# Optimization experiments

Hardware: AMD Instinct MI355X
Metric: run time of the kernel (lower is better)

Reference implementation:

```python
import jax, jax.numpy as jnp
import numpy as np

BS, GRID, A, CH = 32, 2704, 3, 85   # 52x52 YOLO grid, 3 anchors, 80 classes + 5
HW = 52
VDIM, H, SEL = 1024, 512, 32
EPS = 1e-8


def setup_inputs() -> dict:
    key = jax.random.key(0)
    ks = jax.random.split(key, 16)
    s = 0.02
    return {
        "boxes": jax.random.uniform(ks[0], (BS, GRID, A, CH), dtype=jnp.float32),
        "x_feat": jax.random.normal(ks[1], (BS, VDIM, HW, HW), dtype=jnp.float32),
        "tag_emb": jax.random.normal(ks[2], (BS, SEL, H), dtype=jnp.float32),
        "pos_emb": jax.random.normal(ks[3], (BS, SEL, H), dtype=jnp.float32),
        "lang": jax.random.normal(ks[4], (BS, H), dtype=jnp.float32),
        "W_vs": jax.random.normal(ks[5], (VDIM, H), dtype=jnp.float32) * s,
        "b_vs": jnp.zeros((H,), jnp.float32),
        "W_ts": jax.random.normal(ks[6], (H, H), dtype=jnp.float32) * s,
        "b_ts": jnp.zeros((H,), jnp.float32),
        "W_vs_pos": jax.random.normal(ks[7], (H, H), dtype=jnp.float32) * s,
        "b_vs_pos": jnp.zeros((H,), jnp.float32),
        "W_tag": jax.random.normal(ks[8], (H, H), dtype=jnp.float32) * s,
        "b_tag": jnp.zeros((H,), jnp.float32),
        "W_soft": jax.random.normal(ks[9], (H, 2), dtype=jnp.float32) * s,
        "b_soft": jnp.zeros((2,), jnp.float32),
    }


def reference(boxes, x_feat, tag_emb, pos_emb, lang,
              W_vs, b_vs, W_ts, b_ts, W_vs_pos, b_vs_pos,
              W_tag, b_tag, W_soft, b_soft):
    bs = boxes.shape[0]
    # --- topk grid selection on mean objectness (channel 4) ---
    score = jnp.mean(boxes, axis=2)[:, :, 4]                     # [bs, grid]
    _, idx = jax.lax.top_k(score, SEL)                           # [bs, SEL]
    # torch's scatter->masked_select recovers selected grids in ascending
    # index order (not topk-value order), so sort the indices.
    idx = jnp.sort(idx, axis=1)
    # gather selected boxes: [bs, SEL, A, CH]
    boxes_sel = jnp.take_along_axis(boxes, idx[:, :, None, None], axis=1)
    # gather selected visual features: [bs, SEL, VDIM]
    feat = x_feat.reshape(bs, VDIM, -1).transpose(0, 2, 1)       # [bs, grid, VDIM]
    i_sel = jnp.take_along_axis(feat, idx[:, :, None], axis=1)
    # --- gated multimodal fusion ---
    vis = i_sel @ W_vs + b_vs                                    # [bs, SEL, H]
    lang_e = (lang @ W_ts + b_ts)[:, None, :]                    # [bs, 1, H]
    logits = ((vis + tag_emb + pos_emb) @ W_soft + b_soft) / 0.03
    w = jax.nn.log_softmax(logits, axis=-1)                      # [bs, SEL, 2]
    vis2 = ((vis * w[..., 0:1]) @ W_vs_pos + b_vs_pos
            + (tag_emb * w[..., 1:2]) @ W_tag + b_tag
            + pos_emb)                                           # [bs, SEL, H]
    # --- head (eval): cosine similarity vs language, top-1 grid mask ---
    vn = vis2 / (jnp.linalg.norm(vis2, axis=-1, keepdims=True) + EPS)
    ln = lang_e / (jnp.linalg.norm(lang_e, axis=-1, keepdims=True) + EPS)
    sim = jnp.sum(vn * ln, axis=-1)                              # [bs, SEL]
    top_grid = jnp.argmax(sim, axis=1)                           # [bs]
    # --- get_boxes: gather top grid, xywh->xyxy, top-1 box by objectness ---
    sel = jnp.take_along_axis(boxes_sel, top_grid[:, None, None, None], axis=1)
    sel = jax.lax.stop_gradient(sel[:, 0])                       # [bs, A, CH] (.data in torch)
    x1 = sel[..., 0] - sel[..., 2] / 2
    y1 = sel[..., 1] - sel[..., 3] / 2
    x2 = x1 + sel[..., 2]
    y2 = y1 + sel[..., 3]
    bxyxy = jnp.concatenate(
        [jnp.stack([x1, y1, x2, y2], axis=-1), sel[..., 4:]], axis=-1)
    j = jnp.argmax(bxyxy[:, :, 4], axis=1)                       # [bs]
    box_pred = jnp.take_along_axis(bxyxy[:, :, :5], j[:, None, None], axis=1)
    return box_pred, sim
```

## Files before the change

kernel.cpp:

```cpp
#include <hip/hip_runtime.h>
#include <hip/hip_bf16.h>
#include <math.h>

#define BS   32
#define GRID_N 2704
#define A_N  3
#define CH   85
#define VDIM 1024
#define HDIM 512
#define SEL  32
#define ROWS (BS*SEL)

#define WS_VIS   1024
#define WS_VIS2  (WS_VIS + ROWS*HDIM)
#define WS_LN    (WS_VIS2 + ROWS*HDIM)
#define WS_W0    (WS_LN + BS*HDIM)
#define WS_W1    (WS_W0 + ROWS)
#define WS_TOTAL_FLOATS (WS_W1 + ROWS)

__global__ __launch_bounds__(256) void topk_kernel(const float* __restrict__ boxes,
                                                   int* __restrict__ idx_out) {
    __shared__ float sc[GRID_N];
    __shared__ int   selg[SEL];
    __shared__ float rbv[4];
    __shared__ int   rbi[4];
    int b = blockIdx.x, tid = threadIdx.x;
    for (int g = tid; g < GRID_N; g += 256) {
        const float* p = boxes + ((long)(b * GRID_N + g)) * (A_N * CH);
        sc[g] = (p[4] + p[CH + 4] + p[2 * CH + 4]) * (1.0f / 3.0f);
    }
    __syncthreads();
    for (int i = 0; i < SEL; ++i) {
        float bv = -3.4e38f; int bi = 0x7fffffff;
        for (int g = tid; g < GRID_N; g += 256) {
            float v = sc[g];
            if (v > bv || (v == bv && g < bi)) { bv = v; bi = g; }
        }
        for (int off = 32; off; off >>= 1) {
            float ov = __shfl_down(bv, off);
            int   oi = __shfl_down(bi, off);
            if (ov > bv || (ov == bv && oi < bi)) { bv = ov; bi = oi; }
        }
        int lane = tid & 63, wid = tid >> 6;
        if (lane == 0) { rbv[wid] = bv; rbi[wid] = bi; }
        __syncthreads();
        if (tid == 0) {
            float fv = rbv[0]; int fi = rbi[0];
            for (int w = 1; w < 4; ++w)
                if (rbv[w] > fv || (rbv[w] == fv && rbi[w] < fi)) { fv = rbv[w]; fi = rbi[w]; }
            selg[i] = fi;
            sc[fi] = -3.4e38f;
        }
        __syncthreads();
    }
    if (tid < SEL) {
        int my = selg[tid], rank = 0;
        for (int j = 0; j < SEL; ++j) rank += (selg[j] < my);
        idx_out[b * SEL + rank] = my;
    }
}

__global__ __launch_bounds__(256) void lang_kernel(const float* __restrict__ lang,
                                                   const float* __restrict__ Wts,
                                                   const float* __restrict__ bts,
                                                   float* __restrict__ lnorm) {
    __shared__ float ll[HDIM];
    __shared__ float le[HDIM];
    __shared__ float red[4];
    __shared__ float sscale;
    int b = blockIdx.x, tid = threadIdx.x;
    ll[tid]       = lang[b * HDIM + tid];
    ll[tid + 256] = lang[b * HDIM + tid + 256];
    __syncthreads();
    for (int h = tid; h < HDIM; h += 256) {
        float acc = bts[h];
        for (int k = 0; k < HDIM; ++k) acc += ll[k] * Wts[k * HDIM + h];
        le[h] = acc;
    }
    __syncthreads();
    float s = le[tid] * le[tid] + le[tid + 256] * le[tid + 256];
    for (int off = 32; off; off >>= 1) s += __shfl_down(s, off);
    int lane = tid & 63, wid = tid >> 6;
    if (lane == 0) red[wid] = s;
    __syncthreads();
    if (tid == 0) {
        float t = red[0] + red[1] + red[2] + red[3];
        sscale = 1.0f / (sqrtf(t) + 1e-8f);
    }
    __syncthreads();
    lnorm[b * HDIM + tid]       = le[tid] * sscale;
    lnorm[b * HDIM + tid + 256] = le[tid + 256] * sscale;
}

#define KT 256
__global__ __launch_bounds__(256) void gemm1_kernel(const float* __restrict__ xf,
                                                    const int* __restrict__ idx,
                                                    const float* __restrict__ W,
                                                    const float* __restrict__ bias,
                                                    float* __restrict__ out) {
    __shared__ float As[KT][34];
    int tid = threadIdx.x;
    int bx = blockIdx.x, by = blockIdx.y;
    int ct = tid & 15, rt = tid >> 4;
    int c0 = by * 64 + ct * 4;
    int r0 = bx * 32 + rt * 2;
    int lrow = tid >> 3;
    int lk0  = (tid & 7) * 4;
    int g = idx[bx * SEL + lrow];
    const float* src = xf + (long)bx * VDIM * GRID_N + g;
    float acc[2][4] = {{0.f,0.f,0.f,0.f},{0.f,0.f,0.f,0.f}};
    for (int k0 = 0; k0 < VDIM; k0 += KT) {
        #pragma unroll
        for (int j = 0; j < 8; ++j) {
            int kk = lk0 + j * 32;
            #pragma unroll
            for (int i = 0; i < 4; ++i)
                As[kk + i][lrow] = src[(long)(k0 + kk + i) * GRID_N];
        }
        __syncthreads();
        #pragma unroll 8
        for (int k = 0; k < KT; ++k) {
            float4 w = *(const float4*)&W[(long)(k0 + k) * HDIM + c0];
            float2 a = *(const float2*)&As[k][2 * rt];
            acc[0][0] += a.x * w.x; acc[0][1] += a.x * w.y;
            acc[0][2] += a.x * w.z; acc[0][3] += a.x * w.w;
            acc[1][0] += a.y * w.x; acc[1][1] += a.y * w.y;
            acc[1][2] += a.y * w.z; acc[1][3] += a.y * w.w;
        }
        __syncthreads();
    }
    float4 bv = *(const float4*)&bias[c0];
    #pragma unroll
    for (int i = 0; i < 2; ++i) {
        float4 o;
        o.x = acc[i][0] + bv.x; o.y = acc[i][1] + bv.y;
        o.z = acc[i][2] + bv.z; o.w = acc[i][3] + bv.w;
        *(float4*)&out[(long)(r0 + i) * HDIM + c0] = o;
    }
}

__global__ __launch_bounds__(256) void logits_kernel(const float* __restrict__ vis,
                                                     const float* __restrict__ tag,
                                                     const float* __restrict__ pos,
                                                     const float* __restrict__ Wsoft,
                                                     const float* __restrict__ bsoft,
                                                     float* __restrict__ w0,
                                                     float* __restrict__ w1) {
    int tid = threadIdx.x, lane = tid & 63, wid = tid >> 6;
    int r = blockIdx.x * 4 + wid;
    const float* vr = vis + (long)r * HDIM;
    const float* tr = tag + (long)r * HDIM;
    const float* pr = pos + (long)r * HDIM;
    int k = lane * 8;
    float s0 = 0.f, s1 = 0.f;
    #pragma unroll
    for (int j = 0; j < 8; ++j) {
        float t = vr[k + j] + tr[k + j] + pr[k + j];
        s0 += t * Wsoft[(k + j) * 2];
        s1 += t * Wsoft[(k + j) * 2 + 1];
    }
    for (int off = 32; off; off >>= 1) {
        s0 += __shfl_down(s0, off);
        s1 += __shfl_down(s1, off);
    }
    if (lane == 0) {
        float l0 = (s0 + bsoft[0]) / 0.03f;
        float l1 = (s1 + bsoft[1]) / 0.03f;
        float m = fmaxf(l0, l1);
        float lse = m + logf(expf(l0 - m) + expf(l1 - m));
        w0[r] = l0 - lse;
        w1[r] = l1 - lse;
    }
}

__global__ __launch_bounds__(256) void gemm2_kernel(const float* __restrict__ vis,
                                                    const float* __restrict__ tag,
                                                    const float* __restrict__ w0,
                                                    const float* __restrict__ w1,
                                                    const float* __restrict__ Wvp,
                                                    const float* __restrict__ Wtag,
                                                    const float* __restrict__ bvp,
                                                    const float* __restrict__ btag,
                                                    const float* __restrict__ pos,
                                                    float* __restrict__ out) {
    __shared__ float As[KT][34];
    int tid = threadIdx.x;
    int bx = blockIdx.x, by = blockIdx.y;
    int ct = tid & 15, rt = tid >> 4;
    int c0 = by * 64 + ct * 4;
    int r0 = bx * 32 + rt * 2;
    int lrow = tid >> 3;
    int lk0  = (tid & 7) * 4;
    int grow = bx * 32 + lrow;
    float sw0 = w0[grow], sw1 = w1[grow];
    float acc[2][4] = {{0.f,0.f,0.f,0.f},{0.f,0.f,0.f,0.f}};
    for (int k0 = 0; k0 < 2 * HDIM; k0 += KT) {
        #pragma unroll
        for (int j = 0; j < 8; ++j) {
            int kk = lk0 + j * 32;
            int kg = k0 + kk;
            float4 v; float s;
            if (kg < HDIM) {
                v = *(const float4*)&vis[(long)grow * HDIM + kg];
                s = sw0;
            } else {
                v = *(const float4*)&tag[(long)grow * HDIM + kg - HDIM];
                s = sw1;
            }
            As[kk + 0][lrow] = v.x * s; As[kk + 1][lrow] = v.y * s;
            As[kk + 2][lrow] = v.z * s; As[kk + 3][lrow] = v.w * s;
        }
        __syncthreads();
        const float* Wb = (k0 < HDIM) ? (Wvp + (long)k0 * HDIM)
                                      : (Wtag + (long)(k0 - HDIM) * HDIM);
        #pragma unroll 8
        for (int k = 0; k < KT; ++k) {
            float4 w = *(const float4*)&Wb[(long)k * HDIM + c0];
            float2 a = *(const float2*)&As[k][2 * rt];
            acc[0][0] += a.x * w.x; acc[0][1] += a.x * w.y;
            acc[0][2] += a.x * w.z; acc[0][3] += a.x * w.w;
            acc[1][0] += a.y * w.x; acc[1][1] += a.y * w.y;
            acc[1][2] += a.y * w.z; acc[1][3] += a.y * w.w;
        }
        __syncthreads();
    }
    float4 b1 = *(const float4*)&bvp[c0];
    float4 b2 = *(const float4*)&btag[c0];
    #pragma unroll
    for (int i = 0; i < 2; ++i) {
        int r = r0 + i;
        float4 p = *(const float4*)&pos[(long)r * HDIM + c0];
        float4 o;
        o.x = acc[i][0] + b1.x + b2.x + p.x;
        o.y = acc[i][1] + b1.y + b2.y + p.y;
        o.z = acc[i][2] + b1.z + b2.z + p.z;
        o.w = acc[i][3] + b1.w + b2.w + p.w;
        *(float4*)&out[(long)r * HDIM + c0] = o;
    }
}

__global__ __launch_bounds__(256) void final_kernel(const float* __restrict__ vis2,
                                                    const float* __restrict__ lnorm,
                                                    const int* __restrict__ idx,
                                                    const float* __restrict__ boxes,
                                                    float* __restrict__ out) {
    __shared__ float lns[HDIM];
    __shared__ float sims[SEL];
    int b = blockIdx.x, tid = threadIdx.x;
    int lane = tid & 63, wid = tid >> 6;
    lns[tid]       = lnorm[b * HDIM + tid];
    lns[tid + 256] = lnorm[b * HDIM + tid + 256];
    __syncthreads();
    for (int j = 0; j < 8; ++j) {
        int s = wid + j * 4;
        const float* vr = vis2 + (long)(b * SEL + s) * HDIM;
        int k = lane * 8;
        float ss = 0.f, dot = 0.f;
        #pragma unroll
        for (int t = 0; t < 8; ++t) {
            float v = vr[k + t];
            ss += v * v;
            dot += v * lns[k + t];
        }
        for (int off = 32; off; off >>= 1) {
            ss += __shfl_down(ss, off);
            dot += __shfl_down(dot, off);
        }
        if (lane == 0) {
            float sim = dot / (sqrtf(ss) + 1e-8f);
            out[BS * 5 + b * SEL + s] = sim;
            sims[s] = sim;
        }
    }
    __syncthreads();
    if (tid == 0) {
        int bsi = 0; float bvv = sims[0];
        for (int s = 1; s < SEL; ++s)
            if (sims[s] > bvv) { bvv = sims[s]; bsi = s; }
        int g = idx[b * SEL + bsi];
        const float* bb = boxes + ((long)(b * GRID_N + g)) * A_N * CH;
        float o0 = bb[4], o1 = bb[CH + 4], o2 = bb[2 * CH + 4];
        int j = 0; float ov = o0;
        if (o1 > ov) { ov = o1; j = 1; }
        if (o2 > ov) { ov = o2; j = 2; }
        const float* sb = bb + j * CH;
        float x = sb[0], y = sb[1], w = sb[2], h = sb[3];
        float x1 = x - w * 0.5f, y1 = y - h * 0.5f;
        out[b * 5 + 0] = x1;
        out[b * 5 + 1] = y1;
        out[b * 5 + 2] = x1 + w;
        out[b * 5 + 3] = y1 + h;
        out[b * 5 + 4] = sb[4];
    }
}

extern "C" void kernel_launch(void* const* d_in, const int* in_sizes, int n_in,
                              void* d_out, int out_size, void* d_ws, size_t ws_size,
                              hipStream_t stream) {
    const float* boxes    = (const float*)d_in[0];
    const float* x_feat   = (const float*)d_in[1];
    const float* tag_emb  = (const float*)d_in[2];
    const float* pos_emb  = (const float*)d_in[3];
    const float* lang     = (const float*)d_in[4];
    const float* W_vs     = (const float*)d_in[5];
    const float* b_vs     = (const float*)d_in[6];
    const float* W_ts     = (const float*)d_in[7];
    const float* b_ts     = (const float*)d_in[8];
    const float* W_vs_pos = (const float*)d_in[9];
    const float* b_vs_pos = (const float*)d_in[10];
    const float* W_tag    = (const float*)d_in[11];
    const float* b_tag    = (const float*)d_in[12];
    const float* W_soft   = (const float*)d_in[13];
    const float* b_soft   = (const float*)d_in[14];
    float* out = (float*)d_out;

    if (ws_size < (size_t)WS_TOTAL_FLOATS * sizeof(float)) return;

    float* wsf   = (float*)d_ws;
    int*   wsidx = (int*)d_ws;
    float* vis   = wsf + WS_VIS;
    float* vis2  = wsf + WS_VIS2;
    float* ln    = wsf + WS_LN;
    float* w0    = wsf + WS_W0;
    float* w1    = wsf + WS_W1;

    topk_kernel<<<BS, 256, 0, stream>>>(boxes, wsidx);
    lang_kernel<<<BS, 256, 0, stream>>>(lang, W_ts, b_ts, ln);
    gemm1_kernel<<<dim3(32, 8), 256, 0, stream>>>(x_feat, wsidx, W_vs, b_vs, vis);
    logits_kernel<<<ROWS / 4, 256, 0, stream>>>(vis, tag_emb, pos_emb, W_soft, b_soft, w0, w1);
    gemm2_kernel<<<dim3(32, 8), 256, 0, stream>>>(vis, tag_emb, w0, w1, W_vs_pos, W_tag,
                                                  b_vs_pos, b_tag, pos_emb, vis2);
    final_kernel<<<BS, 256, 0, stream>>>(vis2, ln, wsidx, boxes, out);
}
```

Baseline: 750.6 us.

## Split feature gather into own kernel, fuse logits into gemm2 and lang into final

```diff
diff --git a/kernel.cpp b/kernel.cpp
--- a/kernel.cpp
+++ b/kernel.cpp
@@ -11,12 +11,10 @@
 #define SEL  32
 #define ROWS (BS*SEL)
 
-#define WS_VIS   1024
+#define WS_ISEL  1024
+#define WS_VIS   (WS_ISEL + ROWS*VDIM)
 #define WS_VIS2  (WS_VIS + ROWS*HDIM)
-#define WS_LN    (WS_VIS2 + ROWS*HDIM)
-#define WS_W0    (WS_LN + BS*HDIM)
-#define WS_W1    (WS_W0 + ROWS)
-#define WS_TOTAL_FLOATS (WS_W1 + ROWS)
+#define WS_TOTAL_FLOATS (WS_VIS2 + ROWS*HDIM)
 
 __global__ __launch_bounds__(256) void topk_kernel(const float* __restrict__ boxes,
                                                    int* __restrict__ idx_out) {
@@ -60,41 +58,23 @@
     }
 }
 
-__global__ __launch_bounds__(256) void lang_kernel(const float* __restrict__ lang,
-                                                   const float* __restrict__ Wts,
-                                                   const float* __restrict__ bts,
-                                                   float* __restrict__ lnorm) {
-    __shared__ float ll[HDIM];
-    __shared__ float le[HDIM];
-    __shared__ float red[4];
-    __shared__ float sscale;
-    int b = blockIdx.x, tid = threadIdx.x;
-    ll[tid]       = lang[b * HDIM + tid];
-    ll[tid + 256] = lang[b * HDIM + tid + 256];
-    __syncthreads();
-    for (int h = tid; h < HDIM; h += 256) {
-        float acc = bts[h];
-        for (int k = 0; k < HDIM; ++k) acc += ll[k] * Wts[k * HDIM + h];
-        le[h] = acc;
-    }
-    __syncthreads();
-    float s = le[tid] * le[tid] + le[tid + 256] * le[tid + 256];
-    for (int off = 32; off; off >>= 1) s += __shfl_down(s, off);
-    int lane = tid & 63, wid = tid >> 6;
-    if (lane == 0) red[wid] = s;
-    __syncthreads();
-    if (tid == 0) {
-        float t = red[0] + red[1] + red[2] + red[3];
-        sscale = 1.0f / (sqrtf(t) + 1e-8f);
-    }
-    __syncthreads();
-    lnorm[b * HDIM + tid]       = le[tid] * sscale;
-    lnorm[b * HDIM + tid + 256] = le[tid + 256] * sscale;
+__global__ __launch_bounds__(256) void gather_kernel(const float* __restrict__ xf,
+                                                     const int* __restrict__ idx,
+                                                     float* __restrict__ isel) {
+    int r = blockIdx.x;
+    int b = r >> 5;
+    int g = idx[r];
+    const float* src = xf + (long)b * VDIM * GRID_N + g;
+    float* dst = isel + (long)r * VDIM;
+    #pragma unroll
+    for (int j = 0; j < 4; ++j) {
+        int v = threadIdx.x + j * 256;
+        dst[v] = src[(long)v * GRID_N];
+    }
 }
 
 #define KT 256
-__global__ __launch_bounds__(256) void gemm1_kernel(const float* __restrict__ xf,
-                                                    const int* __restrict__ idx,
+__global__ __launch_bounds__(256) void gemm1_kernel(const float* __restrict__ A,
                                                     const float* __restrict__ W,
                                                     const float* __restrict__ bias,
                                                     float* __restrict__ out) {
@@ -106,16 +86,14 @@
     int r0 = bx * 32 + rt * 2;
     int lrow = tid >> 3;
     int lk0  = (tid & 7) * 4;
-    int g = idx[bx * SEL + lrow];
-    const float* src = xf + (long)bx * VDIM * GRID_N + g;
     float acc[2][4] = {{0.f,0.f,0.f,0.f},{0.f,0.f,0.f,0.f}};
     for (int k0 = 0; k0 < VDIM; k0 += KT) {
         #pragma unroll
         for (int j = 0; j < 8; ++j) {
             int kk = lk0 + j * 32;
-            #pragma unroll
-            for (int i = 0; i < 4; ++i)
-                As[kk + i][lrow] = src[(long)(k0 + kk + i) * GRID_N];
+            float4 v = *(const float4*)&A[(long)(bx * 32 + lrow) * VDIM + k0 + kk];
+            As[kk + 0][lrow] = v.x; As[kk + 1][lrow] = v.y;
+            As[kk + 2][lrow] = v.z; As[kk + 3][lrow] = v.w;
         }
         __syncthreads();
         #pragma unroll 8
@@ -139,51 +117,19 @@
     }
 }
 
-__global__ __launch_bounds__(256) void logits_kernel(const float* __restrict__ vis,
-                                                     const float* __restrict__ tag,
-                                                     const float* __restrict__ pos,
-                                                     const float* __restrict__ Wsoft,
-                                                     const float* __restrict__ bsoft,
-                                                     float* __restrict__ w0,
-                                                     float* __restrict__ w1) {
-    int tid = threadIdx.x, lane = tid & 63, wid = tid >> 6;
-    int r = blockIdx.x * 4 + wid;
-    const float* vr = vis + (long)r * HDIM;
-    const float* tr = tag + (long)r * HDIM;
-    const float* pr = pos + (long)r * HDIM;
-    int k = lane * 8;
-    float s0 = 0.f, s1 = 0.f;
-    #pragma unroll
-    for (int j = 0; j < 8; ++j) {
-        float t = vr[k + j] + tr[k + j] + pr[k + j];
-        s0 += t * Wsoft[(k + j) * 2];
-        s1 += t * Wsoft[(k + j) * 2 + 1];
-    }
-    for (int off = 32; off; off >>= 1) {
-        s0 += __shfl_down(s0, off);
-        s1 += __shfl_down(s1, off);
-    }
-    if (lane == 0) {
-        float l0 = (s0 + bsoft[0]) / 0.03f;
-        float l1 = (s1 + bsoft[1]) / 0.03f;
-        float m = fmaxf(l0, l1);
-        float lse = m + logf(expf(l0 - m) + expf(l1 - m));
-        w0[r] = l0 - lse;
-        w1[r] = l1 - lse;
-    }
-}
-
 __global__ __launch_bounds__(256) void gemm2_kernel(const float* __restrict__ vis,
                                                     const float* __restrict__ tag,
-                                                    const float* __restrict__ w0,
-                                                    const float* __restrict__ w1,
+                                                    const float* __restrict__ pos,
+                                                    const float* __restrict__ Wsoft,
+                                                    const float* __restrict__ bsoft,
                                                     const float* __restrict__ Wvp,
                                                     const float* __restrict__ Wtag,
                                                     const float* __restrict__ bvp,
                                                     const float* __restrict__ btag,
-                                                    const float* __restrict__ pos,
                                                     float* __restrict__ out) {
     __shared__ float As[KT][34];
+    __shared__ float w0s[32];
+    __shared__ float w1s[32];
     int tid = threadIdx.x;
     int bx = blockIdx.x, by = blockIdx.y;
     int ct = tid & 15, rt = tid >> 4;
@@ -192,7 +138,41 @@
     int lrow = tid >> 3;
     int lk0  = (tid & 7) * 4;
     int grow = bx * 32 + lrow;
-    float sw0 = w0[grow], sw1 = w1[grow];
+
+    {
+        int sub = tid & 7;
+        const float* vr = vis + (long)grow * HDIM + sub * 64;
+        const float* tr = tag + (long)grow * HDIM + sub * 64;
+        const float* pr = pos + (long)grow * HDIM + sub * 64;
+        const float* wr = Wsoft + (sub * 64) * 2;
+        float s0 = 0.f, s1 = 0.f;
+        #pragma unroll
+        for (int j = 0; j < 16; ++j) {
+            float4 v = *(const float4*)&vr[j * 4];
+            float4 t = *(const float4*)&tr[j * 4];
+            float4 p = *(const float4*)&pr[j * 4];
+            float4 wA = *(const float4*)&wr[j * 8];
+            float4 wB = *(const float4*)&wr[j * 8 + 4];
+            float e0 = v.x + t.x + p.x, e1 = v.y + t.y + p.y;
+            float e2 = v.z + t.z + p.z, e3 = v.w + t.w + p.w;
+            s0 += e0 * wA.x + e1 * wA.z + e2 * wB.x + e3 * wB.z;
+            s1 += e0 * wA.y + e1 * wA.w + e2 * wB.y + e3 * wB.w;
+        }
+        s0 += __shfl_down(s0, 4, 8); s1 += __shfl_down(s1, 4, 8);
+        s0 += __shfl_down(s0, 2, 8); s1 += __shfl_down(s1, 2, 8);
+        s0 += __shfl_down(s0, 1, 8); s1 += __shfl_down(s1, 1, 8);
+        if (sub == 0) {
+            float l0 = (s0 + bsoft[0]) * (1.0f / 0.03f);
+            float l1 = (s1 + bsoft[1]) * (1.0f / 0.03f);
+            float m = fmaxf(l0, l1);
+            float lse = m + logf(expf(l0 - m) + expf(l1 - m));
+            w0s[lrow] = l0 - lse;
+            w1s[lrow] = l1 - lse;
+        }
+    }
+    __syncthreads();
+    float sw0 = w0s[lrow], sw1 = w1s[lrow];
+
     float acc[2][4] = {{0.f,0.f,0.f,0.f},{0.f,0.f,0.f,0.f}};
     for (int k0 = 0; k0 < 2 * HDIM; k0 += KT) {
         #pragma unroll
@@ -240,20 +220,39 @@
 }
 
 __global__ __launch_bounds__(256) void final_kernel(const float* __restrict__ vis2,
-                                                    const float* __restrict__ lnorm,
+                                                    const float* __restrict__ lang,
+                                                    const float* __restrict__ Wts,
+                                                    const float* __restrict__ bts,
                                                     const int* __restrict__ idx,
                                                     const float* __restrict__ boxes,
                                                     float* __restrict__ out) {
+    __shared__ float ll[HDIM];
     __shared__ float lns[HDIM];
+    __shared__ float red[4];
     __shared__ float sims[SEL];
     int b = blockIdx.x, tid = threadIdx.x;
     int lane = tid & 63, wid = tid >> 6;
-    lns[tid]       = lnorm[b * HDIM + tid];
-    lns[tid + 256] = lnorm[b * HDIM + tid + 256];
-    __syncthreads();
+    ll[tid]       = lang[b * HDIM + tid];
+    ll[tid + 256] = lang[b * HDIM + tid + 256];
+    __syncthreads();
+    for (int h = tid; h < HDIM; h += 256) {
+        float acc = bts[h];
+        for (int k = 0; k < HDIM; ++k) acc += ll[k] * Wts[k * HDIM + h];
+        lns[h] = acc;
+    }
+    __syncthreads();
+    float s = lns[tid] * lns[tid] + lns[tid + 256] * lns[tid + 256];
+    for (int off = 32; off; off >>= 1) s += __shfl_down(s, off);
+    if (lane == 0) red[wid] = s;
+    __syncthreads();
+    float sscale;
+    {
+        float t = red[0] + red[1] + red[2] + red[3];
+        sscale = 1.0f / (sqrtf(t) + 1e-8f);
+    }
     for (int j = 0; j < 8; ++j) {
-        int s = wid + j * 4;
-        const float* vr = vis2 + (long)(b * SEL + s) * HDIM;
+        int sl = wid + j * 4;
+        const float* vr = vis2 + (long)(b * SEL + sl) * HDIM;
         int k = lane * 8;
         float ss = 0.f, dot = 0.f;
         #pragma unroll
@@ -267,16 +266,16 @@
             dot += __shfl_down(dot, off);
         }
         if (lane == 0) {
-            float sim = dot / (sqrtf(ss) + 1e-8f);
-            out[BS * 5 + b * SEL + s] = sim;
-            sims[s] = sim;
+            float sim = dot * sscale / (sqrtf(ss) + 1e-8f);
+            out[BS * 5 + b * SEL + sl] = sim;
+            sims[sl] = sim;
         }
     }
     __syncthreads();
     if (tid == 0) {
         int bsi = 0; float bvv = sims[0];
-        for (int s = 1; s < SEL; ++s)
-            if (sims[s] > bvv) { bvv = sims[s]; bsi = s; }
+        for (int sl = 1; sl < SEL; ++sl)
+            if (sims[sl] > bvv) { bvv = sims[sl]; bsi = sl; }
         int g = idx[b * SEL + bsi];
         const float* bb = boxes + ((long)(b * GRID_N + g)) * A_N * CH;
         float o0 = bb[4], o1 = bb[CH + 4], o2 = bb[2 * CH + 4];
@@ -318,17 +317,14 @@
 
     float* wsf   = (float*)d_ws;
     int*   wsidx = (int*)d_ws;
+    float* isel  = wsf + WS_ISEL;
     float* vis   = wsf + WS_VIS;
     float* vis2  = wsf + WS_VIS2;
-    float* ln    = wsf + WS_LN;
-    float* w0    = wsf + WS_W0;
-    float* w1    = wsf + WS_W1;
 
     topk_kernel<<<BS, 256, 0, stream>>>(boxes, wsidx);
-    lang_kernel<<<BS, 256, 0, stream>>>(lang, W_ts, b_ts, ln);
-    gemm1_kernel<<<dim3(32, 8), 256, 0, stream>>>(x_feat, wsidx, W_vs, b_vs, vis);
-    logits_kernel<<<ROWS / 4, 256, 0, stream>>>(vis, tag_emb, pos_emb, W_soft, b_soft, w0, w1);
-    gemm2_kernel<<<dim3(32, 8), 256, 0, stream>>>(vis, tag_emb, w0, w1, W_vs_pos, W_tag,
-                                                  b_vs_pos, b_tag, pos_emb, vis2);
-    final_kernel<<<BS, 256, 0, stream>>>(vis2, ln, wsidx, boxes, out);
-}
+    gather_kernel<<<ROWS, 256, 0, stream>>>(x_feat, wsidx, isel);
+    gemm1_kernel<<<dim3(32, 8), 256, 0, stream>>>(isel, W_vs, b_vs, vis);
+    gemm2_kernel<<<dim3(32, 8), 256, 0, stream>>>(vis, tag_emb, pos_emb, W_soft, b_soft,
+                                                  W_vs_pos, W_tag, b_vs_pos, b_tag, vis2);
+    final_kernel<<<BS, 256, 0, stream>>>(vis2, lang, W_ts, b_ts, wsidx, boxes, out);
+}
```

Result: no change. 755.3 us (+0.6%).
